# Kernel optimization log

Measured on AMD Instinct MI355X. Metric: run time of the kernel, lower is better.

## Reference

```python
import jax, jax.numpy as jnp
import numpy as np

B, C, H, W = 256, 512, 14, 14
HW = H * W
TAU = 0.03          # args.tau
EPS = 0.65          # args.epsilon
EPS2 = 0.40         # args.epsilon - args.epsilon_margin
T_LOGIT = 0.07      # args.logit_temperature
MAX_ITERS = 32      # static unrolled bound for the data-dependent while-loop
PD_EPS = 1e-6       # torch.nn.PairwiseDistance default eps (added to the difference)


def setup_inputs() -> dict:
    key = jax.random.key(0)
    k1, k2 = jax.random.split(key)
    img = jax.random.normal(k1, (B, C, H, W), jnp.float32)
    img = img / (jnp.linalg.norm(img, axis=1, keepdims=True) + 1e-12)  # L2 over channels
    aud = jax.random.normal(k2, (B, C), jnp.float32)
    aud = aud / (jnp.linalg.norm(aud, axis=1, keepdims=True) + 1e-12)
    return {"img": img, "aud": aud}


def reference(img, aud):
    Bb, Cc, Hh, Ww = img.shape
    n_pix = Hh * Ww

    # PosLogits: [B,1,H,W]; Alllogits: [B,B,H,W]
    pos_logits = jnp.einsum('ncqa,nc->nqa', img, aud)[:, None]
    all_logits = jnp.einsum('ncqa,kc->nkqa', img, aud)

    # trimap negatives
    pos2 = jax.nn.sigmoid((pos_logits - EPS2) / TAU)
    neg = 1.0 - pos2                                        # [B,1,H,W]

    logit = img.reshape(Bb, Cc, -1) * pos_logits.reshape(Bb, 1, -1)   # [B,C,HW]
    positive0 = pos_logits.reshape(Bb, -1)                            # [B,HW]
    neg_val = (logit * neg.reshape(Bb, 1, -1)).mean(axis=2)           # [B,C]

    logit_t = logit.transpose(0, 2, 1)                                 # [B,HW,C]
    dist_to_zero = jnp.linalg.norm(logit_t - neg_val[:, None, :] + PD_EPS, axis=-1)  # [B,HW]

    def body(t, state):
        positive, already_pos, endpoint, obj = state
        idx = jnp.argmax(positive, axis=1)                             # [B] (detached in torch)
        sel = jnp.take_along_axis(logit, idx[:, None, None], axis=2)[:, :, 0]  # [B,C]
        obj = obj.at[t].set(sel * (~endpoint)[:, None].astype(sel.dtype))
        dist_to_logit = jnp.linalg.norm(logit_t - sel[:, None, :] + PD_EPS, axis=-1)  # [B,HW]
        pos = (dist_to_logit < dist_to_zero) & (~already_pos)
        already_pos = already_pos | pos
        positive = positive * (1.0 - pos.astype(positive.dtype))
        endpoint = endpoint | (pos.sum(axis=1) == 0) | (positive.max(axis=1) < 0.1)
        return (positive, already_pos, endpoint, obj)

    obj0 = jnp.zeros((MAX_ITERS, Bb, Cc), img.dtype)
    state0 = (positive0,
              jnp.zeros((Bb, n_pix), bool),
              jnp.zeros((Bb,), bool),
              obj0)
    _, _, _, object_arr = jax.lax.fori_loop(0, MAX_ITERS, body, state0)

    # lvs contrastive loss
    mask = 1.0 - 100.0 * jnp.eye(Bb, dtype=img.dtype)
    pos_m = jax.nn.sigmoid((pos_logits - EPS) / TAU)                   # [B,1,H,W]
    pos_all = jax.nn.sigmoid((all_logits - EPS) / TAU)                 # [B,B,H,W]
    sim1 = (pos_m * pos_logits).reshape(Bb, 1, -1).sum(-1) / pos_m.reshape(Bb, 1, -1).sum(-1)
    sim = (pos_all * all_logits).reshape(Bb, Bb, -1).sum(-1) / pos_all.reshape(Bb, Bb, -1).sum(-1) * mask
    sim2 = (neg * pos_logits).reshape(Bb, 1, -1).sum(-1) / neg.reshape(Bb, 1, -1).sum(-1)
    logits = jnp.concatenate((sim1, sim, sim2), axis=1) / T_LOGIT      # [B, B+2]
    loss = -jax.nn.log_softmax(logits, axis=1)[:, 0].mean()           # CE with target 0

    return loss, pos_logits[:, 0], object_arr
```

## Files before the change

kernel.cpp:

```cpp
#include <hip/hip_runtime.h>
#include <hip/hip_bf16.h>
#include <math.h>

#define NB 256
#define NC 512
#define NP 196
#define NIT 32
#define PROWS 208
#define LSTR 72
#define SFSTR 211

typedef __attribute__((ext_vector_type(8))) short bf16x8;
typedef __attribute__((ext_vector_type(4))) float f32x4;

__device__ __forceinline__ float sigf(float z){ return 1.0f/(1.0f+expf(-z)); }

__device__ __forceinline__ unsigned short f2bf(float x){
  return __bfloat16_as_ushort(__float2bfloat16(x));
}
__device__ __forceinline__ float bf2f(unsigned short h){
  union{float f; unsigned u;} v; v.u = ((unsigned)h)<<16; return v.f;
}
__device__ __forceinline__ double dshfl_xor(double v, int m){
  int lo = __shfl_xor(__double2loint(v), m);
  int hi = __shfl_xor(__double2hiint(v), m);
  return __hiloint2double(hi, lo);
}


__global__ __launch_bounds__(512) void convert4_kernel(
    const float* __restrict__ img, const float* __restrict__ aud,
    unsigned short* __restrict__ hiT, unsigned short* __restrict__ loT,
    unsigned short* __restrict__ aud_bf,
    double* __restrict__ ppl, double* __restrict__ pcs)
{
  const int bid = blockIdx.x;
  const int b = bid & 255, part = bid >> 8;
  const int tid = threadIdx.x;
  const float* imgb = img + (size_t)b*NC*NP + (size_t)part*64*NP;
  __shared__ float sf[64*SFSTR];
  __shared__ float s_aud[64];
  if (part == 0) aud_bf[b*NC + tid] = f2bf(aud[b*NC + tid]);
  if (tid < 64) s_aud[tid] = aud[b*NC + part*64 + tid];

  for (int j=tid; j<64*49; j+=512){
    int p4 = j % 49, c = j / 49;
    float4 v = *(const float4*)&imgb[(size_t)c*NP + p4*4];
    sf[c*SFSTR + p4*4+0]=v.x; sf[c*SFSTR + p4*4+1]=v.y;
    sf[c*SFSTR + p4*4+2]=v.z; sf[c*SFSTR + p4*4+3]=v.w;
  }
  __syncthreads();

  unsigned short* hp = hiT + (size_t)(b*8+part)*PROWS*64;
  unsigned short* lp = loT + (size_t)(b*8+part)*PROWS*64;
  for (int j=tid; j<PROWS*8; j+=512){
    int p = j>>3, o = j&7;
    unsigned hw[4], lw[4];
    double dot=0.0, sm=0.0;
    #pragma unroll
    for (int k2=0;k2<4;++k2){
      int c = o*8 + 2*k2;
      float x0 = (p<NP) ? sf[c*SFSTR + p]     : 0.f;
      float x1 = (p<NP) ? sf[(c+1)*SFSTR + p] : 0.f;
      unsigned short h0=f2bf(x0), h1=f2bf(x1);
      unsigned short l0=f2bf(x0-bf2f(h0)), l1=f2bf(x1-bf2f(h1));
      hw[k2] = (unsigned)h0 | ((unsigned)h1<<16);
      lw[k2] = (unsigned)l0 | ((unsigned)l1<<16);
      dot += (double)x0*(double)s_aud[c] + (double)x1*(double)s_aud[c+1];
      sm  += (double)x0 + (double)x1;
    }
    if (p < NP){
      *(uint4*)&hp[p*64 + o*8] = *(uint4*)hw;
      *(uint4*)&lp[p*64 + o*8] = *(uint4*)lw;
    }
    dot += dshfl_xor(dot,1); dot += dshfl_xor(dot,2); dot += dshfl_xor(dot,4);
    sm  += dshfl_xor(sm,1);  sm  += dshfl_xor(sm,2);  sm  += dshfl_xor(sm,4);
    if (o==0 && p<NP){
      ppl[(size_t)(b*8+part)*NP + p] = dot;
      pcs[(size_t)(b*8+part)*NP + p] = sm;
    }
  }
}

__global__ __launch_bounds__(256) void prep3_kernel(
    const double* __restrict__ ppl, const double* __restrict__ pcs,
    float* __restrict__ pl, float* __restrict__ cs,
    float* __restrict__ sim1, float* __restrict__ sim2, float* __restrict__ out_pl)
{
  const int b = blockIdx.x, tid = threadIdx.x;
  __shared__ double s_redd[256];
  float plv=0.f;
  if (tid < NP){
    double a=0.0, s=0.0;
    #pragma unroll
    for (int part=0; part<8; ++part){
      a += ppl[(size_t)(b*8+part)*NP + tid];
      s += pcs[(size_t)(b*8+part)*NP + tid];
    }
    plv=(float)a;
    float csv=(float)s;
    pl[b*NP+tid]=plv; cs[b*NP+tid]=csv; out_pl[b*NP+tid]=plv;
  }
  float pmw = (tid<NP)? sigf((plv-0.65f)/0.03f) : 0.f;
  float negw= (tid<NP)? 1.0f - sigf((plv-0.40f)/0.03f) : 0.f;
  double r[4];
  r[0]=(tid<NP)?(double)pmw*(double)plv:0.0;
  r[1]=(tid<NP)?(double)pmw:0.0;
  r[2]=(tid<NP)?(double)negw*(double)plv:0.0;
  r[3]=(tid<NP)?(double)negw:0.0;
  double res[4];
  for (int i=0;i<4;++i){
    __syncthreads();
    s_redd[tid]=r[i];
    __syncthreads();
    for (int s=128;s>0;s>>=1){ if (tid<s) s_redd[tid]+=s_redd[tid+s]; __syncthreads(); }
    res[i]=s_redd[0];
  }
  if (tid==0){
    sim1[b]=(float)(res[0]/res[1]);
    sim2[b]=(float)(res[2]/res[3]);
  }
}

__global__ __launch_bounds__(512) void gram2_kernel(
    const unsigned short* __restrict__ hiT, const unsigned short* __restrict__ loT,
    float* __restrict__ G)
{
  const int bid = blockIdx.x;
  const int slot = bid & 7, seq = bid >> 3;
  const int b = slot + 8*(seq>>1), h = seq & 1;
  const int cbase = 7*h, ncl = 7 - h;
  const int tid = threadIdx.x, lane = tid & 63, w = tid >> 6;
  const int nr = (w<5)?2:1;
  const unsigned short* hb = hiT + (size_t)b*8*PROWS*64;
  const unsigned short* lb = loT + (size_t)b*8*PROWS*64;
  float* Gb = G + (size_t)b*NP*NP;
  __shared__ short smh[PROWS*LSTR];
  __shared__ short sml[PROWS*LSTR];

  f32x4 acc[2][7];
  #pragma unroll
  for (int i=0;i<2;++i)
    #pragma unroll
    for (int j=0;j<7;++j) acc[i][j]=(f32x4){0,0,0,0};

  for (int sl=0; sl<8; ++sl){
    __syncthreads();
    for (int j=tid; j<PROWS*8; j+=512){
      int p = j>>3, o = j&7;
      size_t src = ((size_t)sl*PROWS + p)*64 + o*8;
      *(uint4*)&smh[p*LSTR + o*8] = *(const uint4*)(hb + src);
      *(uint4*)&sml[p*LSTR + o*8] = *(const uint4*)(lb + src);
    }
    __syncthreads();
    #pragma unroll
    for (int kk=0; kk<2; ++kk){
      bf16x8 Ah[2], Al[2];
      #pragma unroll
      for (int i=0;i<2;++i){
        if (i<nr){
          int r = (w + 8*i)*16 + (lane&15);
          Ah[i] = *(const bf16x8*)&smh[r*LSTR + kk*32 + (lane>>4)*8];
          Al[i] = *(const bf16x8*)&sml[r*LSTR + kk*32 + (lane>>4)*8];
        }
      }
      #pragma unroll
      for (int j=0;j<7;++j){
        if (j<ncl){
          int r = (cbase+j)*16 + (lane&15);
          bf16x8 Bh = *(const bf16x8*)&smh[r*LSTR + kk*32 + (lane>>4)*8];
          bf16x8 Bl = *(const bf16x8*)&sml[r*LSTR + kk*32 + (lane>>4)*8];
          #pragma unroll
          for (int i=0;i<2;++i){
            if (i<nr){
              acc[i][j] = __builtin_amdgcn_mfma_f32_16x16x32_bf16(Ah[i], Bh, acc[i][j], 0,0,0);
              acc[i][j] = __builtin_amdgcn_mfma_f32_16x16x32_bf16(Ah[i], Bl, acc[i][j], 0,0,0);
              acc[i][j] = __builtin_amdgcn_mfma_f32_16x16x32_bf16(Al[i], Bh, acc[i][j], 0,0,0);
            }
          }
        }
      }
    }
  }

  const int r0 = (lane>>4)*4, colL = lane & 15;
  #pragma unroll
  for (int i=0;i<2;++i){
    #pragma unroll
    for (int j=0;j<7;++j){
      if (i<nr && j<ncl){
        int row = (w+8*i)*16 + r0;
        int col = (cbase+j)*16 + colL;
        if (col < NP){
          #pragma unroll
          for (int jj=0;jj<4;++jj){
            if (row+jj < NP) Gb[(size_t)(row+jj)*NP + col] = acc[i][j][jj];
          }
        }
      }
    }
  }
}

__global__ __launch_bounds__(512) void simgemm2_kernel(
    const unsigned short* __restrict__ hiT, const unsigned short* __restrict__ aud_bf,
    float* __restrict__ sumWA, float* __restrict__ sumW)
{
  const int bid = blockIdx.x;
  const int slot = bid & 7, seq = bid >> 3;
  const int b = slot + 8*(seq>>1), h = seq & 1;
  const int tid = threadIdx.x, lane = tid & 63, w = tid >> 6;
  const int wr = w >> 2, wc = w & 3;
  const int pbase = (wr==0)?0:7, npt = 7-wr;
  const unsigned short* hb = hiT + (size_t)b*8*PROWS*64;
  __shared__ short smh[PROWS*LSTR];
  __shared__ short sma[128*LSTR];
  __shared__ float sred[2][2][4][2][16];

  f32x4 acc[7][2];
  #pragma unroll
  for (int i=0;i<7;++i)
    #pragma unroll
    for (int n=0;n<2;++n) acc[i][n]=(f32x4){0,0,0,0};

  for (int sl=0; sl<8; ++sl){
    __syncthreads();
    for (int j=tid; j<PROWS*8; j+=512){
      int p = j>>3, o = j&7;
      *(uint4*)&smh[p*LSTR + o*8] = *(const uint4*)(hb + ((size_t)sl*PROWS + p)*64 + o*8);
    }
    for (int j=tid; j<128*8; j+=512){
      int n = j>>3, o = j&7;
      *(uint4*)&sma[n*LSTR + o*8] = *(const uint4*)(aud_bf + (size_t)(h*128+n)*NC + sl*64 + o*8);
    }
    __syncthreads();
    #pragma unroll
    for (int kk=0; kk<2; ++kk){
      bf16x8 Ah[7];
      #pragma unroll
      for (int i=0;i<7;++i){
        if (i<npt){
          int r = (pbase+i)*16 + (lane&15);
          Ah[i] = *(const bf16x8*)&smh[r*LSTR + kk*32 + (lane>>4)*8];
        }
      }
      #pragma unroll
      for (int n=0;n<2;++n){
        int r = (wc*2+n)*16 + (lane&15);
        bf16x8 Bn = *(const bf16x8*)&sma[r*LSTR + kk*32 + (lane>>4)*8];
        #pragma unroll
        for (int i=0;i<7;++i)
          if (i<npt)
            acc[i][n] = __builtin_amdgcn_mfma_f32_16x16x32_bf16(Ah[i], Bn, acc[i][n], 0,0,0);
      }
    }
  }

  float swa[2]={0,0}, sw[2]={0,0};
  #pragma unroll
  for (int n=0;n<2;++n){
    #pragma unroll
    for (int i=0;i<7;++i){
      if (i<npt){
        int rowbase = (pbase+i)*16 + (lane>>4)*4;
        #pragma unroll
        for (int jj=0;jj<4;++jj){
          if (rowbase+jj < NP){
            float v = acc[i][n][jj];
            float wgt = sigf((v-0.65f)/0.03f);
            swa[n] += wgt*v; sw[n] += wgt;
          }
        }
      }
    }
  }
  #pragma unroll
  for (int n=0;n<2;++n){
    swa[n] += __shfl_xor(swa[n],16); swa[n] += __shfl_xor(swa[n],32);
    sw[n]  += __shfl_xor(sw[n],16);  sw[n]  += __shfl_xor(sw[n],32);
  }
  if (lane < 16){
    #pragma unroll
    for (int n=0;n<2;++n){
      sred[0][wr][wc][n][lane] = swa[n];
      sred[1][wr][wc][n][lane] = sw[n];
    }
  }
  __syncthreads();
  if (tid < 128){
    int wc2 = tid>>5, n2 = (tid>>4)&1, col = tid&15;
    float a = sred[0][0][wc2][n2][col] + sred[0][1][wc2][n2][col];
    float s = sred[1][0][wc2][n2][col] + sred[1][1][wc2][n2][col];
    int kcol = h*128 + (wc2*2+n2)*16 + col;
    sumWA[(size_t)b*NB + kcol] = a;
    sumW [(size_t)b*NB + kcol] = s;
  }
}

__global__ __launch_bounds__(1024) void loop5_kernel(
    const float* __restrict__ pl, const float* __restrict__ cs,
    const float* __restrict__ G,
    const unsigned short* __restrict__ hiT, const unsigned short* __restrict__ loT,
    float* __restrict__ obj)
{
  const int b = blockIdx.x, tid = threadIdx.x, lane = tid & 63, w = tid >> 6;
  const float* Gb = G + (size_t)b*NP*NP;
  __shared__ float sG[NP*NP];
  __shared__ float s_pl[NP], s_wl[NP], s_csL[NP], s_gd[NP];
  __shared__ double gwd[NP];
  __shared__ double s_wred[16];
  __shared__ double s_bc;
  __shared__ int s_q[NIT]; __shared__ int s_z[NIT];

  #pragma unroll
  for (int k=0;k<10;++k){
    int j = k*1024 + tid;
    if (j < NP*NP/4) ((float4*)sG)[j] = ((const float4*)Gb)[j];
  }
  float negw_t = 0.f;
  if (tid < NP){
    float plv = pl[b*NP+tid];
    float csv = cs[b*NP+tid];
    s_pl[tid] = plv;
    s_csL[tid] = plv*csv;
    negw_t = 1.0f - sigf((plv-0.40f)/0.03f);
    s_wl[tid] = plv*negw_t;
    s_gd[tid] = Gb[(size_t)tid*NP + tid];
  }
  __syncthreads();

  {
    int p = tid >> 2, qg = tid & 3;
    double a = 0.0;
    if (p < NP){
      for (int q=qg*49; q<qg*49+49; ++q) a += (double)sG[q*NP + p] * (double)s_wl[q];
    }
    a += dshfl_xor(a,1); a += dshfl_xor(a,2);
    if (qg==0 && p<NP) gwd[p] = a;
  }
  __syncthreads();

  double r = (tid<NP) ? (double)s_wl[tid]*gwd[tid] : 0.0;
  #pragma unroll
  for (int m=1;m<64;m<<=1) r += dshfl_xor(r,m);
  if (lane==0) s_wred[w] = r;
  __syncthreads();
  if (tid==0){ double t=0.0; for (int i=0;i<16;++i) t += s_wred[i]; s_bc = t; }
  __syncthreads();
  const double S2 = s_bc;
  __syncthreads();

  r = (tid<NP) ? (double)negw_t*(double)s_csL[tid] : 0.0;
  #pragma unroll
  for (int m=1;m<64;m<<=1) r += dshfl_xor(r,m);
  if (lane==0) s_wred[w] = r;
  __syncthreads();
  if (tid==0){ double t=0.0; for (int i=0;i<16;++i) t += s_wred[i]; s_bc = t; }
  __syncthreads();
  const double Swl = s_bc;
  __syncthreads();

  if (tid < NP){
    const double e = (double)1e-6f;
    double pld = (double)s_pl[tid];
    double d0sq = pld*pld*(double)s_gd[tid]
                - (2.0/196.0)*pld*gwd[tid]
                + S2/(196.0*196.0)
                + 2.0*e*((double)s_csL[tid] - Swl/196.0)
                + 512.0*e*e;
    if (d0sq < 0.0) d0sq = 0.0;
    gwd[tid] = d0sq;
  }
  __syncthreads();

  if (w == 0){
    float plv[4], csL[4], gdd[4], posv[4];
    double d0sq[4];
    bool alr[4];
    #pragma unroll
    for (int s=0;s<4;++s){
      int p = lane + 64*s;
      bool valid = p < NP;
      plv[s]  = valid ? s_pl[p]  : 0.f;
      csL[s]  = valid ? s_csL[p] : 0.f;
      gdd[s]  = valid ? s_gd[p]  : 0.f;
      d0sq[s] = valid ? gwd[p]   : 0.0;
      posv[s] = valid ? plv[s]   : -INFINITY;
      alr[s] = false;
    }
    bool endp = false;

    for (int t=0;t<NIT;++t){
      float v = posv[0]; int ix = lane;
      #pragma unroll
      for (int s=1;s<4;++s){
        if (posv[s] > v){ v = posv[s]; ix = lane + 64*s; }
      }
      #pragma unroll
      for (int m=1;m<64;m<<=1){
        float vv = __shfl_xor(v, m);
        int   ii = __shfl_xor(ix, m);
        if (vv>v || (vv==v && ii<ix)){ v=vv; ix=ii; }
      }
      const int q = ix;
      const float plq  = s_pl[q];
      const float gqq  = s_gd[q];
      const float csLq = s_csL[q];
      if (lane==0){ s_q[t] = q; s_z[t] = endp ? 1 : 0; }

      int cnt = 0;
      #pragma unroll
      for (int s=0;s<4;++s){
        int p = lane + 64*s;
        if (p<NP && !alr[s]){
          float Gpq = sG[q*NP + p];
          double plp=(double)plv[s], dq=(double)plq;
          const double e=(double)1e-6f;
          double d2 = plp*plp*(double)gdd[s]
                    - 2.0*plp*dq*(double)Gpq
                    + dq*dq*(double)gqq
                    + 2.0*e*((double)csL[s]-(double)csLq)
                    + 512.0*e*e;
          if (d2<0.0) d2=0.0;
          if (d2 < d0sq[s]){ alr[s]=true; posv[s]=posv[s]*0.0f; cnt++; }
        }
      }
      float mx = fmaxf(fmaxf(posv[0],posv[1]),fmaxf(posv[2],posv[3]));
      #pragma unroll
      for (int m=1;m<64;m<<=1){
        cnt += __shfl_xor(cnt, m);
        mx = fmaxf(mx, __shfl_xor(mx, m));
      }
      if (cnt==0 || mx<0.1f) endp=true;
    }
  }
  __syncthreads();

  for (int j=tid; j<NIT*64; j+=1024){
    int t = j >> 6, l8 = j & 63;
    int part = l8 >> 3, off = l8 & 7;
    float o8[8];
    if (s_z[t]){
      #pragma unroll
      for (int e=0;e<8;++e) o8[e]=0.f;
    } else {
      int q = s_q[t];
      float plq = s_pl[q];
      size_t src = ((size_t)(b*8+part)*PROWS + q)*64 + off*8;
      uint4 hv = *(const uint4*)(hiT + src);
      uint4 lv = *(const uint4*)(loT + src);
      const unsigned* hw = (const unsigned*)&hv;
      const unsigned* lw = (const unsigned*)&lv;
      #pragma unroll
      for (int k2=0;k2<4;++k2){
        float x0 = bf2f((unsigned short)(hw[k2]&0xffff)) + bf2f((unsigned short)(lw[k2]&0xffff));
        float x1 = bf2f((unsigned short)(hw[k2]>>16))    + bf2f((unsigned short)(lw[k2]>>16));
        o8[2*k2]   = x0*plq;
        o8[2*k2+1] = x1*plq;
      }
    }
    float* op = obj + ((size_t)t*NB + b)*NC + l8*8;
    *(float4*)&op[0] = *(float4*)&o8[0];
    *(float4*)&op[4] = *(float4*)&o8[4];
  }
}

__global__ __launch_bounds__(256) void finalize_b(
    const float* __restrict__ sim1, const float* __restrict__ sim2,
    const float* __restrict__ sumWA, const float* __restrict__ sumW,
    float* __restrict__ lossb)
{
  const int b = blockIdx.x, k = threadIdx.x;
  __shared__ float s_red[256];
  __shared__ double s_redd[256];
  const float T = 0.07f;
  float s = sumWA[(size_t)b*NB+k]/sumW[(size_t)b*NB+k];
  if (k==b) s *= -99.0f;
  const float lk = s/T;
  const float l0 = sim1[b]/T, ll = sim2[b]/T;
  s_red[k]=lk; __syncthreads();
  for (int st=128;st>0;st>>=1){ if(k<st) s_red[k]=fmaxf(s_red[k],s_red[k+st]); __syncthreads(); }
  const float m = fmaxf(s_red[0], fmaxf(l0,ll));
  __syncthreads();
  double e = (double)expf(lk-m);
  if (k==0) e += (double)expf(l0-m)+(double)expf(ll-m);
  s_redd[k]=e; __syncthreads();
  for (int st=128;st>0;st>>=1){ if(k<st) s_redd[k]+=s_redd[k+st]; __syncthreads(); }
  if (k==0) lossb[b] = -(float)((double)(l0-m) - log(s_redd[0]));
}

__global__ __launch_bounds__(256) void finalize_sum(const float* __restrict__ lossb, float* __restrict__ out_loss)
{
  const int tid = threadIdx.x;
  __shared__ double sr[256];
  sr[tid]=(double)lossb[tid]; __syncthreads();
  for (int st=128;st>0;st>>=1){ if(tid<st) sr[tid]+=sr[tid+st]; __syncthreads(); }
  if (tid==0) out_loss[0]=(float)(sr[0]/256.0);
}

extern "C" void kernel_launch(void* const* d_in, const int* in_sizes, int n_in,
                              void* d_out, int out_size, void* d_ws, size_t ws_size,
                              hipStream_t stream)
{
  const float* img = (const float*)d_in[0];
  const float* aud = (const float*)d_in[1];
  float* out = (float*)d_out;
  float* ws  = (float*)d_ws;

  float* pl    = ws;
  float* cs    = pl    + NB*NP;
  float* sim1  = cs    + NB*NP;
  float* sim2  = sim1  + NB;
  float* sumWA = sim2  + NB;
  float* sumW  = sumWA + NB*NB;
  unsigned short* aud_bf = (unsigned short*)(sumW + NB*NB);
  float* G     = (float*)(aud_bf + NB*NC);
  unsigned short* hiT = (unsigned short*)(G + (size_t)NB*NP*NP);
  unsigned short* loT = hiT + (size_t)NB*8*PROWS*64;
  float* lossb = (float*)(loT + (size_t)NB*8*PROWS*64);

  double* ppl = (double*)G;
  double* pcs = ppl + (size_t)NB*8*NP;

  float* out_loss = out;
  float* out_pl   = out + 1;
  float* out_obj  = out + 1 + NB*NP;

  hipLaunchKernelGGL(convert4_kernel, dim3(NB*8),  dim3(512),  0, stream, img, aud, hiT, loT, aud_bf, ppl, pcs);
  hipLaunchKernelGGL(prep3_kernel,    dim3(NB),    dim3(256),  0, stream, ppl, pcs, pl, cs, sim1, sim2, out_pl);
  hipLaunchKernelGGL(gram2_kernel,    dim3(NB*2),  dim3(512),  0, stream, hiT, loT, G);
  hipLaunchKernelGGL(loop5_kernel,    dim3(NB),    dim3(1024), 0, stream, pl, cs, G, hiT, loT, out_obj);
  hipLaunchKernelGGL(simgemm2_kernel, dim3(NB*2),  dim3(512),  0, stream, hiT, aud_bf, sumWA, sumW);
  hipLaunchKernelGGL(finalize_b,      dim3(NB),    dim3(256),  0, stream, sim1, sim2, sumWA, sumW, lossb);
  hipLaunchKernelGGL(finalize_sum,    dim3(1),     dim3(256),  0, stream, lossb, out_loss);
}
```

Baseline: 191.7 us.

## Fuse Gram-matrix GEMM and greedy selection loop into one per-batch kernel

Merges prep3, gram2 and loop5 into a single 1024-thread kernel per batch. It computes the 196x196 Gram matrix with MFMA, writes it straight into shared memory and runs the greedy selection loop there, so the G matrix no longer goes through global memory. The sim1/sim2 reductions move into the finalize kernel. The costs are one block per batch for the GEMM (256 blocks instead of 512) with 13 of 16 waves busy, and a larger shared-memory footprint that may limit occupancy.

```diff
diff --git a/kernel.cpp b/kernel.cpp
--- a/kernel.cpp
+++ b/kernel.cpp
@@ -82,14 +82,27 @@
   }
 }
 
-__global__ __launch_bounds__(256) void prep3_kernel(
+__global__ __launch_bounds__(1024) void gramloop_kernel(
+    const unsigned short* __restrict__ hiT, const unsigned short* __restrict__ loT,
     const double* __restrict__ ppl, const double* __restrict__ pcs,
-    float* __restrict__ pl, float* __restrict__ cs,
-    float* __restrict__ sim1, float* __restrict__ sim2, float* __restrict__ out_pl)
-{
-  const int b = blockIdx.x, tid = threadIdx.x;
-  __shared__ double s_redd[256];
-  float plv=0.f;
+    float* __restrict__ pl, float* __restrict__ out_pl,
+    float* __restrict__ obj)
+{
+  const int b = blockIdx.x, tid = threadIdx.x, lane = tid & 63, w = tid >> 6;
+  const unsigned short* hb = hiT + (size_t)b*8*PROWS*64;
+  const unsigned short* lb = loT + (size_t)b*8*PROWS*64;
+
+  __shared__ union {
+    struct { short smh[PROWS*LSTR]; short sml[PROWS*LSTR]; } st;
+    float sG[NP*NP];
+  } u;
+  __shared__ float s_pl[NP], s_wl[NP], s_csL[NP], s_gd[NP];
+  __shared__ double gwd[NP];
+  __shared__ double s_wred[16];
+  __shared__ double s_bc;
+  __shared__ int s_q[NIT]; __shared__ int s_z[NIT];
+
+  float negw_t = 0.f;
   if (tid < NP){
     double a=0.0, s=0.0;
     #pragma unroll
@@ -97,108 +110,200 @@
       a += ppl[(size_t)(b*8+part)*NP + tid];
       s += pcs[(size_t)(b*8+part)*NP + tid];
     }
-    plv=(float)a;
+    float plv=(float)a;
     float csv=(float)s;
-    pl[b*NP+tid]=plv; cs[b*NP+tid]=csv; out_pl[b*NP+tid]=plv;
-  }
-  float pmw = (tid<NP)? sigf((plv-0.65f)/0.03f) : 0.f;
-  float negw= (tid<NP)? 1.0f - sigf((plv-0.40f)/0.03f) : 0.f;
-  double r[4];
-  r[0]=(tid<NP)?(double)pmw*(double)plv:0.0;
-  r[1]=(tid<NP)?(double)pmw:0.0;
-  r[2]=(tid<NP)?(double)negw*(double)plv:0.0;
-  r[3]=(tid<NP)?(double)negw:0.0;
-  double res[4];
-  for (int i=0;i<4;++i){
-    __syncthreads();
-    s_redd[tid]=r[i];
-    __syncthreads();
-    for (int s=128;s>0;s>>=1){ if (tid<s) s_redd[tid]+=s_redd[tid+s]; __syncthreads(); }
-    res[i]=s_redd[0];
-  }
-  if (tid==0){
-    sim1[b]=(float)(res[0]/res[1]);
-    sim2[b]=(float)(res[2]/res[3]);
-  }
-}
-
-__global__ __launch_bounds__(512) void gram2_kernel(
-    const unsigned short* __restrict__ hiT, const unsigned short* __restrict__ loT,
-    float* __restrict__ G)
-{
-  const int bid = blockIdx.x;
-  const int slot = bid & 7, seq = bid >> 3;
-  const int b = slot + 8*(seq>>1), h = seq & 1;
-  const int cbase = 7*h, ncl = 7 - h;
-  const int tid = threadIdx.x, lane = tid & 63, w = tid >> 6;
-  const int nr = (w<5)?2:1;
-  const unsigned short* hb = hiT + (size_t)b*8*PROWS*64;
-  const unsigned short* lb = loT + (size_t)b*8*PROWS*64;
-  float* Gb = G + (size_t)b*NP*NP;
-  __shared__ short smh[PROWS*LSTR];
-  __shared__ short sml[PROWS*LSTR];
-
-  f32x4 acc[2][7];
-  #pragma unroll
-  for (int i=0;i<2;++i)
-    #pragma unroll
-    for (int j=0;j<7;++j) acc[i][j]=(f32x4){0,0,0,0};
+    pl[b*NP+tid]=plv; out_pl[b*NP+tid]=plv;
+    s_pl[tid] = plv;
+    s_csL[tid] = plv*csv;
+    negw_t = 1.0f - sigf((plv-0.40f)/0.03f);
+    s_wl[tid] = plv*negw_t;
+  }
+
+  f32x4 acc[13];
+  #pragma unroll
+  for (int j=0;j<13;++j) acc[j]=(f32x4){0,0,0,0};
 
   for (int sl=0; sl<8; ++sl){
     __syncthreads();
-    for (int j=tid; j<PROWS*8; j+=512){
+    for (int j=tid; j<PROWS*8; j+=1024){
       int p = j>>3, o = j&7;
       size_t src = ((size_t)sl*PROWS + p)*64 + o*8;
-      *(uint4*)&smh[p*LSTR + o*8] = *(const uint4*)(hb + src);
-      *(uint4*)&sml[p*LSTR + o*8] = *(const uint4*)(lb + src);
-    }
-    __syncthreads();
-    #pragma unroll
-    for (int kk=0; kk<2; ++kk){
-      bf16x8 Ah[2], Al[2];
-      #pragma unroll
-      for (int i=0;i<2;++i){
-        if (i<nr){
-          int r = (w + 8*i)*16 + (lane&15);
-          Ah[i] = *(const bf16x8*)&smh[r*LSTR + kk*32 + (lane>>4)*8];
-          Al[i] = *(const bf16x8*)&sml[r*LSTR + kk*32 + (lane>>4)*8];
+      *(uint4*)&u.st.smh[p*LSTR + o*8] = *(const uint4*)(hb + src);
+      *(uint4*)&u.st.sml[p*LSTR + o*8] = *(const uint4*)(lb + src);
+    }
+    __syncthreads();
+    if (w < 13){
+      #pragma unroll
+      for (int kk=0; kk<2; ++kk){
+        int r = w*16 + (lane&15);
+        bf16x8 Ah = *(const bf16x8*)&u.st.smh[r*LSTR + kk*32 + (lane>>4)*8];
+        bf16x8 Al = *(const bf16x8*)&u.st.sml[r*LSTR + kk*32 + (lane>>4)*8];
+        #pragma unroll
+        for (int j=0;j<13;++j){
+          int rc = j*16 + (lane&15);
+          bf16x8 Bh = *(const bf16x8*)&u.st.smh[rc*LSTR + kk*32 + (lane>>4)*8];
+          bf16x8 Bl = *(const bf16x8*)&u.st.sml[rc*LSTR + kk*32 + (lane>>4)*8];
+          acc[j] = __builtin_amdgcn_mfma_f32_16x16x32_bf16(Ah, Bh, acc[j], 0,0,0);
+          acc[j] = __builtin_amdgcn_mfma_f32_16x16x32_bf16(Ah, Bl, acc[j], 0,0,0);
+          acc[j] = __builtin_amdgcn_mfma_f32_16x16x32_bf16(Al, Bh, acc[j], 0,0,0);
         }
       }
-      #pragma unroll
-      for (int j=0;j<7;++j){
-        if (j<ncl){
-          int r = (cbase+j)*16 + (lane&15);
-          bf16x8 Bh = *(const bf16x8*)&smh[r*LSTR + kk*32 + (lane>>4)*8];
-          bf16x8 Bl = *(const bf16x8*)&sml[r*LSTR + kk*32 + (lane>>4)*8];
-          #pragma unroll
-          for (int i=0;i<2;++i){
-            if (i<nr){
-              acc[i][j] = __builtin_amdgcn_mfma_f32_16x16x32_bf16(Ah[i], Bh, acc[i][j], 0,0,0);
-              acc[i][j] = __builtin_amdgcn_mfma_f32_16x16x32_bf16(Ah[i], Bl, acc[i][j], 0,0,0);
-              acc[i][j] = __builtin_amdgcn_mfma_f32_16x16x32_bf16(Al[i], Bh, acc[i][j], 0,0,0);
-            }
-          }
+    }
+  }
+  __syncthreads();
+
+  if (w < 13){
+    const int r0 = (lane>>4)*4, colL = lane & 15;
+    #pragma unroll
+    for (int j=0;j<13;++j){
+      int col = j*16 + colL;
+      if (col < NP){
+        #pragma unroll
+        for (int jj=0;jj<4;++jj){
+          int row = w*16 + r0 + jj;
+          if (row < NP) u.sG[row*NP + col] = acc[j][jj];
         }
       }
     }
   }
-
-  const int r0 = (lane>>4)*4, colL = lane & 15;
-  #pragma unroll
-  for (int i=0;i<2;++i){
-    #pragma unroll
-    for (int j=0;j<7;++j){
-      if (i<nr && j<ncl){
-        int row = (w+8*i)*16 + r0;
-        int col = (cbase+j)*16 + colL;
-        if (col < NP){
-          #pragma unroll
-          for (int jj=0;jj<4;++jj){
-            if (row+jj < NP) Gb[(size_t)(row+jj)*NP + col] = acc[i][j][jj];
-          }
+  __syncthreads();
+
+  if (tid < NP) s_gd[tid] = u.sG[tid*NP + tid];
+  __syncthreads();
+
+  {
+    int p = tid >> 2, qg = tid & 3;
+    double a = 0.0;
+    if (p < NP){
+      for (int q=qg*49; q<qg*49+49; ++q) a += (double)u.sG[q*NP + p] * (double)s_wl[q];
+    }
+    a += dshfl_xor(a,1); a += dshfl_xor(a,2);
+    if (qg==0 && p<NP) gwd[p] = a;
+  }
+  __syncthreads();
+
+  double r = (tid<NP) ? (double)s_wl[tid]*gwd[tid] : 0.0;
+  #pragma unroll
+  for (int m=1;m<64;m<<=1) r += dshfl_xor(r,m);
+  if (lane==0) s_wred[w] = r;
+  __syncthreads();
+  if (tid==0){ double t=0.0; for (int i=0;i<16;++i) t += s_wred[i]; s_bc = t; }
+  __syncthreads();
+  const double S2 = s_bc;
+  __syncthreads();
+
+  r = (tid<NP) ? (double)negw_t*(double)s_csL[tid] : 0.0;
+  #pragma unroll
+  for (int m=1;m<64;m<<=1) r += dshfl_xor(r,m);
+  if (lane==0) s_wred[w] = r;
+  __syncthreads();
+  if (tid==0){ double t=0.0; for (int i=0;i<16;++i) t += s_wred[i]; s_bc = t; }
+  __syncthreads();
+  const double Swl = s_bc;
+  __syncthreads();
+
+  if (tid < NP){
+    const double e = (double)1e-6f;
+    double pld = (double)s_pl[tid];
+    double d0sq = pld*pld*(double)s_gd[tid]
+                - (2.0/196.0)*pld*gwd[tid]
+                + S2/(196.0*196.0)
+                + 2.0*e*((double)s_csL[tid] - Swl/196.0)
+                + 512.0*e*e;
+    if (d0sq < 0.0) d0sq = 0.0;
+    gwd[tid] = d0sq;
+  }
+  __syncthreads();
+
+  if (w == 0){
+    float plv[4], csL[4], gdd[4], posv[4];
+    double d0sq[4];
+    bool alr[4];
+    #pragma unroll
+    for (int s=0;s<4;++s){
+      int p = lane + 64*s;
+      bool valid = p < NP;
+      plv[s]  = valid ? s_pl[p]  : 0.f;
+      csL[s]  = valid ? s_csL[p] : 0.f;
+      gdd[s]  = valid ? s_gd[p]  : 0.f;
+      d0sq[s] = valid ? gwd[p]   : 0.0;
+      posv[s] = valid ? plv[s]   : -INFINITY;
+      alr[s] = false;
+    }
+    bool endp = false;
+
+    for (int t=0;t<NIT;++t){
+      float v = posv[0]; int ix = lane;
+      #pragma unroll
+      for (int s=1;s<4;++s){
+        if (posv[s] > v){ v = posv[s]; ix = lane + 64*s; }
+      }
+      #pragma unroll
+      for (int m=1;m<64;m<<=1){
+        float vv = __shfl_xor(v, m);
+        int   ii = __shfl_xor(ix, m);
+        if (vv>v || (vv==v && ii<ix)){ v=vv; ix=ii; }
+      }
+      const int q = ix;
+      const float plq  = s_pl[q];
+      const float gqq  = s_gd[q];
+      const float csLq = s_csL[q];
+      if (lane==0){ s_q[t] = q; s_z[t] = endp ? 1 : 0; }
+
+      int cnt = 0;
+      #pragma unroll
+      for (int s=0;s<4;++s){
+        int p = lane + 64*s;
+        if (p<NP && !alr[s]){
+          float Gpq = u.sG[q*NP + p];
+          double plp=(double)plv[s], dq=(double)plq;
+          const double e=(double)1e-6f;
+          double d2 = plp*plp*(double)gdd[s]
+                    - 2.0*plp*dq*(double)Gpq
+                    + dq*dq*(double)gqq
+                    + 2.0*e*((double)csL[s]-(double)csLq)
+                    + 512.0*e*e;
+          if (d2<0.0) d2=0.0;
+          if (d2 < d0sq[s]){ alr[s]=true; posv[s]=posv[s]*0.0f; cnt++; }
         }
       }
-    }
+      float mx = fmaxf(fmaxf(posv[0],posv[1]),fmaxf(posv[2],posv[3]));
+      #pragma unroll
+      for (int m=1;m<64;m<<=1){
+        cnt += __shfl_xor(cnt, m);
+        mx = fmaxf(mx, __shfl_xor(mx, m));
+      }
+      if (cnt==0 || mx<0.1f) endp=true;
+    }
+  }
+  __syncthreads();
+
+  for (int j=tid; j<NIT*64; j+=1024){
+    int t = j >> 6, l8 = j & 63;
+    int part = l8 >> 3, off = l8 & 7;
+    float o8[8];
+    if (s_z[t]){
+      #pragma unroll
+      for (int e=0;e<8;++e) o8[e]=0.f;
+    } else {
+      int q = s_q[t];
+      float plq = s_pl[q];
+      size_t src = ((size_t)(b*8+part)*PROWS + q)*64 + off*8;
+      uint4 hv = *(const uint4*)(hiT + src);
+      uint4 lv = *(const uint4*)(loT + src);
+      const unsigned* hw = (const unsigned*)&hv;
+      const unsigned* lw = (const unsigned*)&lv;
+      #pragma unroll
+      for (int k2=0;k2<4;++k2){
+        float x0 = bf2f((unsigned short)(hw[k2]&0xffff)) + bf2f((unsigned short)(lw[k2]&0xffff));
+        float x1 = bf2f((unsigned short)(hw[k2]>>16))    + bf2f((unsigned short)(lw[k2]>>16));
+        o8[2*k2]   = x0*plq;
+        o8[2*k2+1] = x1*plq;
+      }
+    }
+    float* op = obj + ((size_t)t*NB + b)*NC + l8*8;
+    *(float4*)&op[0] = *(float4*)&o8[0];
+    *(float4*)&op[4] = *(float4*)&o8[4];
   }
 }
 
@@ -297,187 +402,40 @@
   }
 }
 
-__global__ __launch_bounds__(1024) void loop5_kernel(
-    const float* __restrict__ pl, const float* __restrict__ cs,
-    const float* __restrict__ G,
-    const unsigned short* __restrict__ hiT, const unsigned short* __restrict__ loT,
-    float* __restrict__ obj)
-{
-  const int b = blockIdx.x, tid = threadIdx.x, lane = tid & 63, w = tid >> 6;
-  const float* Gb = G + (size_t)b*NP*NP;
-  __shared__ float sG[NP*NP];
-  __shared__ float s_pl[NP], s_wl[NP], s_csL[NP], s_gd[NP];
-  __shared__ double gwd[NP];
-  __shared__ double s_wred[16];
-  __shared__ double s_bc;
-  __shared__ int s_q[NIT]; __shared__ int s_z[NIT];
-
-  #pragma unroll
-  for (int k=0;k<10;++k){
-    int j = k*1024 + tid;
-    if (j < NP*NP/4) ((float4*)sG)[j] = ((const float4*)Gb)[j];
-  }
-  float negw_t = 0.f;
-  if (tid < NP){
-    float plv = pl[b*NP+tid];
-    float csv = cs[b*NP+tid];
-    s_pl[tid] = plv;
-    s_csL[tid] = plv*csv;
-    negw_t = 1.0f - sigf((plv-0.40f)/0.03f);
-    s_wl[tid] = plv*negw_t;
-    s_gd[tid] = Gb[(size_t)tid*NP + tid];
-  }
-  __syncthreads();
-
-  {
-    int p = tid >> 2, qg = tid & 3;
-    double a = 0.0;
-    if (p < NP){
-      for (int q=qg*49; q<qg*49+49; ++q) a += (double)sG[q*NP + p] * (double)s_wl[q];
-    }
-    a += dshfl_xor(a,1); a += dshfl_xor(a,2);
-    if (qg==0 && p<NP) gwd[p] = a;
-  }
-  __syncthreads();
-
-  double r = (tid<NP) ? (double)s_wl[tid]*gwd[tid] : 0.0;
-  #pragma unroll
-  for (int m=1;m<64;m<<=1) r += dshfl_xor(r,m);
-  if (lane==0) s_wred[w] = r;
-  __syncthreads();
-  if (tid==0){ double t=0.0; for (int i=0;i<16;++i) t += s_wred[i]; s_bc = t; }
-  __syncthreads();
-  const double S2 = s_bc;
-  __syncthreads();
-
-  r = (tid<NP) ? (double)negw_t*(double)s_csL[tid] : 0.0;
-  #pragma unroll
-  for (int m=1;m<64;m<<=1) r += dshfl_xor(r,m);
-  if (lane==0) s_wred[w] = r;
-  __syncthreads();
-  if (tid==0){ double t=0.0; for (int i=0;i<16;++i) t += s_wred[i]; s_bc = t; }
-  __syncthreads();
-  const double Swl = s_bc;
-  __syncthreads();
-
-  if (tid < NP){
-    const double e = (double)1e-6f;
-    double pld = (double)s_pl[tid];
-    double d0sq = pld*pld*(double)s_gd[tid]
-                - (2.0/196.0)*pld*gwd[tid]
-                + S2/(196.0*196.0)
-                + 2.0*e*((double)s_csL[tid] - Swl/196.0)
-                + 512.0*e*e;
-    if (d0sq < 0.0) d0sq = 0.0;
-    gwd[tid] = d0sq;
-  }
-  __syncthreads();
-
-  if (w == 0){
-    float plv[4], csL[4], gdd[4], posv[4];
-    double d0sq[4];
-    bool alr[4];
-    #pragma unroll
-    for (int s=0;s<4;++s){
-      int p = lane + 64*s;
-      bool valid = p < NP;
-      plv[s]  = valid ? s_pl[p]  : 0.f;
-      csL[s]  = valid ? s_csL[p] : 0.f;
-      gdd[s]  = valid ? s_gd[p]  : 0.f;
-      d0sq[s] = valid ? gwd[p]   : 0.0;
-      posv[s] = valid ? plv[s]   : -INFINITY;
-      alr[s] = false;
-    }
-    bool endp = false;
-
-    for (int t=0;t<NIT;++t){
-      float v = posv[0]; int ix = lane;
-      #pragma unroll
-      for (int s=1;s<4;++s){
-        if (posv[s] > v){ v = posv[s]; ix = lane + 64*s; }
-      }
-      #pragma unroll
-      for (int m=1;m<64;m<<=1){
-        float vv = __shfl_xor(v, m);
-        int   ii = __shfl_xor(ix, m);
-        if (vv>v || (vv==v && ii<ix)){ v=vv; ix=ii; }
-      }
-      const int q = ix;
-      const float plq  = s_pl[q];
-      const float gqq  = s_gd[q];
-      const float csLq = s_csL[q];
-      if (lane==0){ s_q[t] = q; s_z[t] = endp ? 1 : 0; }
-
-      int cnt = 0;
-      #pragma unroll
-      for (int s=0;s<4;++s){
-        int p = lane + 64*s;
-        if (p<NP && !alr[s]){
-          float Gpq = sG[q*NP + p];
-          double plp=(double)plv[s], dq=(double)plq;
-          const double e=(double)1e-6f;
-          double d2 = plp*plp*(double)gdd[s]
-                    - 2.0*plp*dq*(double)Gpq
-                    + dq*dq*(double)gqq
-                    + 2.0*e*((double)csL[s]-(double)csLq)
-                    + 512.0*e*e;
-          if (d2<0.0) d2=0.0;
-          if (d2 < d0sq[s]){ alr[s]=true; posv[s]=posv[s]*0.0f; cnt++; }
-        }
-      }
-      float mx = fmaxf(fmaxf(posv[0],posv[1]),fmaxf(posv[2],posv[3]));
-      #pragma unroll
-      for (int m=1;m<64;m<<=1){
-        cnt += __shfl_xor(cnt, m);
-        mx = fmaxf(mx, __shfl_xor(mx, m));
-      }
-      if (cnt==0 || mx<0.1f) endp=true;
-    }
-  }
-  __syncthreads();
-
-  for (int j=tid; j<NIT*64; j+=1024){
-    int t = j >> 6, l8 = j & 63;
-    int part = l8 >> 3, off = l8 & 7;
-    float o8[8];
-    if (s_z[t]){
-      #pragma unroll
-      for (int e=0;e<8;++e) o8[e]=0.f;
-    } else {
-      int q = s_q[t];
-      float plq = s_pl[q];
-      size_t src = ((size_t)(b*8+part)*PROWS + q)*64 + off*8;
-      uint4 hv = *(const uint4*)(hiT + src);
-      uint4 lv = *(const uint4*)(loT + src);
-      const unsigned* hw = (const unsigned*)&hv;
-      const unsigned* lw = (const unsigned*)&lv;
-      #pragma unroll
-      for (int k2=0;k2<4;++k2){
-        float x0 = bf2f((unsigned short)(hw[k2]&0xffff)) + bf2f((unsigned short)(lw[k2]&0xffff));
-        float x1 = bf2f((unsigned short)(hw[k2]>>16))    + bf2f((unsigned short)(lw[k2]>>16));
-        o8[2*k2]   = x0*plq;
-        o8[2*k2+1] = x1*plq;
-      }
-    }
-    float* op = obj + ((size_t)t*NB + b)*NC + l8*8;
-    *(float4*)&op[0] = *(float4*)&o8[0];
-    *(float4*)&op[4] = *(float4*)&o8[4];
-  }
-}
-
-__global__ __launch_bounds__(256) void finalize_b(
-    const float* __restrict__ sim1, const float* __restrict__ sim2,
+__global__ __launch_bounds__(256) void finalize_b2(
+    const float* __restrict__ pl,
     const float* __restrict__ sumWA, const float* __restrict__ sumW,
     float* __restrict__ lossb)
 {
   const int b = blockIdx.x, k = threadIdx.x;
   __shared__ float s_red[256];
   __shared__ double s_redd[256];
+
+  float plv = (k<NP)? pl[b*NP+k] : 0.f;
+  float pmw = (k<NP)? sigf((plv-0.65f)/0.03f) : 0.f;
+  float negw= (k<NP)? 1.0f - sigf((plv-0.40f)/0.03f) : 0.f;
+  double rr[4];
+  rr[0]=(k<NP)?(double)pmw*(double)plv:0.0;
+  rr[1]=(k<NP)?(double)pmw:0.0;
+  rr[2]=(k<NP)?(double)negw*(double)plv:0.0;
+  rr[3]=(k<NP)?(double)negw:0.0;
+  double res[4];
+  for (int i=0;i<4;++i){
+    __syncthreads();
+    s_redd[k]=rr[i];
+    __syncthreads();
+    for (int s=128;s>0;s>>=1){ if (k<s) s_redd[k]+=s_redd[k+s]; __syncthreads(); }
+    res[i]=s_redd[0];
+  }
+  const float sim1v = (float)(res[0]/res[1]);
+  const float sim2v = (float)(res[2]/res[3]);
+  __syncthreads();
+
   const float T = 0.07f;
   float s = sumWA[(size_t)b*NB+k]/sumW[(size_t)b*NB+k];
   if (k==b) s *= -99.0f;
   const float lk = s/T;
-  const float l0 = sim1[b]/T, ll = sim2[b]/T;
+  const float l0 = sim1v/T, ll = sim2v/T;
   s_red[k]=lk; __syncthreads();
   for (int st=128;st>0;st>>=1){ if(k<st) s_red[k]=fmaxf(s_red[k],s_red[k+st]); __syncthreads(); }
   const float m = fmaxf(s_red[0], fmaxf(l0,ll));
@@ -508,29 +466,22 @@
   float* ws  = (float*)d_ws;
 
   float* pl    = ws;
-  float* cs    = pl    + NB*NP;
-  float* sim1  = cs    + NB*NP;
-  float* sim2  = sim1  + NB;
-  float* sumWA = sim2  + NB;
+  float* sumWA = pl    + NB*NP;
   float* sumW  = sumWA + NB*NB;
   unsigned short* aud_bf = (unsigned short*)(sumW + NB*NB);
-  float* G     = (float*)(aud_bf + NB*NC);
-  unsigned short* hiT = (unsigned short*)(G + (size_t)NB*NP*NP);
+  unsigned short* hiT = (unsigned short*)(aud_bf + NB*NC);
   unsigned short* loT = hiT + (size_t)NB*8*PROWS*64;
-  float* lossb = (float*)(loT + (size_t)NB*8*PROWS*64);
-
-  double* ppl = (double*)G;
-  double* pcs = ppl + (size_t)NB*8*NP;
+  double* ppl  = (double*)(loT + (size_t)NB*8*PROWS*64);
+  double* pcs  = ppl + (size_t)NB*8*NP;
+  float* lossb = (float*)(pcs + (size_t)NB*8*NP);
 
   float* out_loss = out;
   float* out_pl   = out + 1;
   float* out_obj  = out + 1 + NB*NP;
 
   hipLaunchKernelGGL(convert4_kernel, dim3(NB*8),  dim3(512),  0, stream, img, aud, hiT, loT, aud_bf, ppl, pcs);
-  hipLaunchKernelGGL(prep3_kernel,    dim3(NB),    dim3(256),  0, stream, ppl, pcs, pl, cs, sim1, sim2, out_pl);
-  hipLaunchKernelGGL(gram2_kernel,    dim3(NB*2),  dim3(512),  0, stream, hiT, loT, G);
-  hipLaunchKernelGGL(loop5_kernel,    dim3(NB),    dim3(1024), 0, stream, pl, cs, G, hiT, loT, out_obj);
+  hipLaunchKernelGGL(gramloop_kernel, dim3(NB),    dim3(1024), 0, stream, hiT, loT, ppl, pcs, pl, out_pl, out_obj);
   hipLaunchKernelGGL(simgemm2_kernel, dim3(NB*2),  dim3(512),  0, stream, hiT, aud_bf, sumWA, sumW);
-  hipLaunchKernelGGL(finalize_b,      dim3(NB),    dim3(256),  0, stream, sim1, sim2, sumWA, sumW, lossb);
+  hipLaunchKernelGGL(finalize_b2,     dim3(NB),    dim3(256),  0, stream, pl, sumWA, sumW, lossb);
   hipLaunchKernelGGL(finalize_sum,    dim3(1),     dim3(256),  0, stream, lossb, out_loss);
 }
```

Result: slower. 229.1 us (+19.5%).
